# Performance work log

Measured on AMD Instinct MI355X. Metric: run time of the kernel, lower is better.

The kernel has to match this reference:

```python
import jax, jax.numpy as jnp
import numpy as np

SPARSITY = 0.01
NUM_BLOCKS = 8

def _softshrink(v, lam):
    return jnp.sign(v) * jnp.maximum(jnp.abs(v) - lam, 0.0)

def setup_inputs() -> dict:
    key = jax.random.key(0)
    ks = jax.random.split(key, 5)
    B, H, W, C = 4, 128, 128, 768
    nb, bs = NUM_BLOCKS, C // NUM_BLOCKS
    return {
        "x": jax.random.normal(ks[0], (B, H, W, C), dtype=jnp.float32),
        "w1": jax.random.normal(ks[1], (2, nb, bs, bs), dtype=jnp.float32) * 0.02,
        "b1": jax.random.normal(ks[2], (2, nb, bs), dtype=jnp.float32) * 0.02,
        "w2": jax.random.normal(ks[3], (2, nb, bs, bs), dtype=jnp.float32) * 0.02,
        "b2": jax.random.normal(ks[4], (2, nb, bs), dtype=jnp.float32) * 0.02,
    }

def reference(x, w1, b1, w2, b2):
    B, H, W, C = x.shape
    nb = NUM_BLOCKS
    bs = C // nb
    # FFT token mixing (ortho-normalized), real->complex half-spectrum
    xf = jnp.fft.rfft2(x, axes=(1, 2), norm="ortho")  # [B, H, W//2+1, C]
    Hf, Wf = xf.shape[1], xf.shape[2]
    xr = xf.real.reshape(B, Hf, Wf, nb, bs)
    xi = xf.imag.reshape(B, Hf, Wf, nb, bs)
    # kept_modes = H*W//2+1 with hard_thresholding_fraction=1 >= Wf -> all modes kept
    # Block-diagonal complex MLP layer 1 + GELU (exact, matching torch nn.GELU)
    o1r = jax.nn.gelu(
        jnp.einsum("bhwni,nio->bhwno", xr, w1[0])
        - jnp.einsum("bhwni,nio->bhwno", xi, w1[1]) + b1[0],
        approximate=False)
    o1i = jax.nn.gelu(
        jnp.einsum("bhwni,nio->bhwno", xi, w1[0])
        + jnp.einsum("bhwni,nio->bhwno", xr, w1[1]) + b1[1],
        approximate=False)
    # Layer 2 (complex matmul), then softshrink on real/imag parts
    o2r = (jnp.einsum("bhwni,nio->bhwno", o1r, w2[0])
           - jnp.einsum("bhwni,nio->bhwno", o1i, w2[1]) + b2[0])
    o2i = (jnp.einsum("bhwni,nio->bhwno", o1i, w2[0])
           + jnp.einsum("bhwni,nio->bhwno", o1r, w2[1]) + b2[1])
    o2r = _softshrink(o2r, SPARSITY)
    o2i = _softshrink(o2i, SPARSITY)
    xc = (o2r + 1j * o2i).reshape(B, Hf, Wf, C)
    out = jnp.fft.irfft2(xc, s=(H, W), axes=(1, 2), norm="ortho")
    return out
```

## Files before the change

### kernel.cpp

```cpp
#include <hip/hip_runtime.h>
#include <hip/hip_bf16.h>
#include <math.h>

typedef __bf16 bfx8 __attribute__((ext_vector_type(8)));
typedef __bf16 bfx4 __attribute__((ext_vector_type(4)));
typedef float f32x4 __attribute__((ext_vector_type(4)));

__device__ __forceinline__ int bitrev7(int x) {
  return ((x & 1) << 6) | ((x & 2) << 4) | ((x & 4) << 2) | (x & 8)
       | ((x & 16) >> 2) | ((x & 32) >> 4) | ((x & 64) >> 6);
}

__device__ __forceinline__ void bfly(float& ar, float& ai, float& br, float& bi,
                                     float tc, float ts) {
  float dr = ar - br, di = ai - bi;
  ar += br; ai += bi;
  br = dr * tc - di * ts;
  bi = dr * ts + di * tc;
}

__device__ __forceinline__ void build_tw(float2* tw, float sign, int tid) {
  if (tid < 64) {
    float s_, c_;
    __sincosf(sign * (float)(2.0 * M_PI / 128.0) * (float)tid, &s_, &c_);
    tw[tid] = make_float2(c_, s_);
  }
}

__device__ __forceinline__ void fft_stages04(float (&xr)[4][8], float (&xi)[4][8],
                                             const float2* tw, int wq) {
  #pragma unroll
  for (int a = 0; a < 8; ++a) {
    #pragma unroll
    for (int b = 0; b < 2; ++b) {
      float2 t = tw[wq + 4 * a + 32 * b];
      bfly(xr[b][a], xi[b][a], xr[b + 2][a], xi[b + 2][a], t.x, t.y);
    }
  }
  #pragma unroll
  for (int a = 0; a < 8; ++a) {
    float2 t = tw[2 * (wq + 4 * a)];
    bfly(xr[0][a], xi[0][a], xr[1][a], xi[1][a], t.x, t.y);
    bfly(xr[2][a], xi[2][a], xr[3][a], xi[3][a], t.x, t.y);
  }
  #pragma unroll
  for (int a = 0; a < 4; ++a) {
    float2 t = tw[4 * (wq + 4 * a)];
    #pragma unroll
    for (int b = 0; b < 4; ++b)
      bfly(xr[b][a], xi[b][a], xr[b][a + 4], xi[b][a + 4], t.x, t.y);
  }
  {
    float2 t0 = tw[8 * wq];
    float2 t1 = tw[8 * (wq + 4)];
    #pragma unroll
    for (int b = 0; b < 4; ++b) {
      bfly(xr[b][0], xi[b][0], xr[b][2], xi[b][2], t0.x, t0.y);
      bfly(xr[b][1], xi[b][1], xr[b][3], xi[b][3], t1.x, t1.y);
      bfly(xr[b][4], xi[b][4], xr[b][6], xi[b][6], t0.x, t0.y);
      bfly(xr[b][5], xi[b][5], xr[b][7], xi[b][7], t1.x, t1.y);
    }
  }
  {
    float2 t = tw[16 * wq];
    #pragma unroll
    for (int b = 0; b < 4; ++b) {
      #pragma unroll
      for (int a = 0; a < 8; a += 2)
        bfly(xr[b][a], xi[b][a], xr[b][a + 1], xi[b][a + 1], t.x, t.y);
    }
  }
}

__device__ __forceinline__ void fft_stages56(float (&yr)[4], float (&yi)[4], float sign) {
  float dr, di;
  dr = yr[0] - yr[2]; di = yi[0] - yi[2];
  yr[0] += yr[2]; yi[0] += yi[2]; yr[2] = dr; yi[2] = di;
  dr = yr[1] - yr[3]; di = yi[1] - yi[3];
  yr[1] += yr[3]; yi[1] += yi[3];
  yr[3] = -sign * di; yi[3] = sign * dr;
  dr = yr[0] - yr[1]; di = yi[0] - yi[1];
  yr[0] += yr[1]; yi[0] += yi[1]; yr[1] = dr; yi[1] = di;
  dr = yr[2] - yr[3]; di = yi[2] - yi[3];
  yr[2] += yr[3]; yi[2] += yi[3]; yr[3] = dr; yi[3] = di;
}

__global__ __launch_bounds__(256, 2) void k_fftw_fwd(
    const float* __restrict__ x, float* __restrict__ Xr, float* __restrict__ Xi) {
  __shared__ float2 l[128 * 64];
  __shared__ float2 tw[64];
  const int bh = blockIdx.x;
  const int c0 = blockIdx.y * 64;
  const int tid = threadIdx.x;
  const int c = tid & 63, wq = tid >> 6;
  build_tw(tw, -1.f, tid);
  const float* xrow = x + (size_t)bh * (128 * 768) + c0 + c;
  float xr[4][8], xi_[4][8];
  #pragma unroll
  for (int b = 0; b < 4; ++b)
    #pragma unroll
    for (int a = 0; a < 8; ++a) {
      int p = wq + 4 * a + 32 * b;
      xr[b][a] = xrow[(size_t)p * 768];
      xi_[b][a] = 0.f;
    }
  __syncthreads();
  fft_stages04(xr, xi_, tw, wq);
  #pragma unroll
  for (int b = 0; b < 4; ++b)
    #pragma unroll
    for (int a = 0; a < 8; ++a) {
      int p = wq + 4 * a + 32 * b;
      l[p * 64 + c] = make_float2(xr[b][a], xi_[b][a]);
    }
  __syncthreads();
  const float sc = 1.f / 128.f;
  #pragma unroll
  for (int t = 0; t < 8; ++t) {
    int g = wq + 4 * t;
    float yr[4], yi[4];
    #pragma unroll
    for (int d = 0; d < 4; ++d) {
      float2 v = l[(4 * g + d) * 64 + c];
      yr[d] = v.x; yi[d] = v.y;
    }
    fft_stages56(yr, yi, -1.f);
    #pragma unroll
    for (int d = 0; d < 4; ++d) {
      int f = bitrev7(4 * g + d);
      if (f < 65) {
        Xr[((size_t)bh * 65 + f) * 768 + c0 + c]  = yr[d] * sc;
        Xi[((size_t)bh * 128 + f) * 768 + c0 + c] = yi[d] * sc;
      }
    }
  }
}

__global__ __launch_bounds__(256, 2) void k_ffth(
    float* Xr, float* Xi, float sign, float scale) {
  __shared__ float2 l[128 * 64];
  __shared__ float2 tw[64];
  const int bw = blockIdx.x;
  const int b = bw / 65, wf = bw % 65;
  const int c0 = blockIdx.y * 64;
  const int tid = threadIdx.x;
  const int c = tid & 63, wq = tid >> 6;
  build_tw(tw, sign, tid);
  const size_t baser = ((size_t)b * 128 * 65 + wf) * 768 + c0 + c;
  const size_t basei = ((size_t)b * 128 * 128 + wf) * 768 + c0 + c;
  float xr[4][8], xi_[4][8];
  #pragma unroll
  for (int bb = 0; bb < 4; ++bb)
    #pragma unroll
    for (int a = 0; a < 8; ++a) {
      int p = wq + 4 * a + 32 * bb;
      xr[bb][a]  = Xr[baser + (size_t)p * (65 * 768)];
      xi_[bb][a] = Xi[basei + (size_t)p * (128 * 768)];
    }
  __syncthreads();
  fft_stages04(xr, xi_, tw, wq);
  #pragma unroll
  for (int bb = 0; bb < 4; ++bb)
    #pragma unroll
    for (int a = 0; a < 8; ++a) {
      int p = wq + 4 * a + 32 * bb;
      l[p * 64 + c] = make_float2(xr[bb][a], xi_[bb][a]);
    }
  __syncthreads();
  #pragma unroll
  for (int t = 0; t < 8; ++t) {
    int g = wq + 4 * t;
    float yr[4], yi[4];
    #pragma unroll
    for (int d = 0; d < 4; ++d) {
      float2 v = l[(4 * g + d) * 64 + c];
      yr[d] = v.x; yi[d] = v.y;
    }
    fft_stages56(yr, yi, sign);
    #pragma unroll
    for (int d = 0; d < 4; ++d) {
      int hf = bitrev7(4 * g + d);
      Xr[baser + (size_t)hf * (65 * 768)]  = yr[d] * scale;
      Xi[basei + (size_t)hf * (128 * 768)] = yi[d] * scale;
    }
  }
}

#define MP 104
__device__ __forceinline__ bfx8 neg8(bfx8 v) {
  union { bfx8 b; unsigned int u[4]; } t;
  t.b = v;
  t.u[0] ^= 0x80008000u; t.u[1] ^= 0x80008000u;
  t.u[2] ^= 0x80008000u; t.u[3] ^= 0x80008000u;
  return t.b;
}

__global__ __launch_bounds__(256, 2) void k_mlp(
    float* __restrict__ Xr, float* __restrict__ Xi,
    const float* __restrict__ w1, const float* __restrict__ b1,
    const float* __restrict__ w2, const float* __restrict__ b2) {
  __shared__ __align__(16) __bf16 Xl[2][64][MP];
  __shared__ __align__(16) __bf16 Wl[2][96][MP];
  const int n = blockIdx.y;
  const int m0 = blockIdx.x * 64;
  const int tid = threadIdx.x;
  const int lane = tid & 63;
  const int w = tid >> 6;
  const int col = lane & 15;
  const int quad = lane >> 4;

  for (int e = tid; e < 64 * 24; e += 256) {
    int mm = e / 24, k4 = (e % 24) * 4;
    int m = m0 + mm;
    int bh = m / 65, wf = m - bh * 65;
    const float4 vr = *(const float4*)&Xr[(size_t)m * 768 + n * 96 + k4];
    const float4 vi = *(const float4*)&Xi[((size_t)bh * 128 + wf) * 768 + n * 96 + k4];
    bfx4 br = { (__bf16)vr.x, (__bf16)vr.y, (__bf16)vr.z, (__bf16)vr.w };
    bfx4 bi = { (__bf16)vi.x, (__bf16)vi.y, (__bf16)vi.z, (__bf16)vi.w };
    *(bfx4*)&Xl[0][mm][k4] = br;
    *(bfx4*)&Xl[1][mm][k4] = bi;
  }
  for (int e = tid; e < 2 * 96 * 24; e += 256) {
    int ri = e / (96 * 24);
    int r = e - ri * (96 * 24);
    int kin = r / 24, oc4 = (r - kin * 24) * 4;
    const float4 v = *(const float4*)&w1[(size_t)ri * 73728 + ((size_t)n * 96 + kin) * 96 + oc4];
    Wl[ri][oc4 + 0][kin] = (__bf16)v.x;
    Wl[ri][oc4 + 1][kin] = (__bf16)v.y;
    Wl[ri][oc4 + 2][kin] = (__bf16)v.z;
    Wl[ri][oc4 + 3][kin] = (__bf16)v.w;
  }
  __syncthreads();

  const f32x4 fz = { 0.f, 0.f, 0.f, 0.f };
  f32x4 accR[6], accI[6];
  #pragma unroll
  for (int ct = 0; ct < 6; ++ct) { accR[ct] = fz; accI[ct] = fz; }

  const int mrow = w * 16 + col;
  #pragma unroll
  for (int kc = 0; kc < 3; ++kc) {
    const int kb = kc * 32 + quad * 8;
    bfx8 axr = *(const bfx8*)&Xl[0][mrow][kb];
    bfx8 axi = *(const bfx8*)&Xl[1][mrow][kb];
    bfx8 axin = neg8(axi);
    #pragma unroll
    for (int ct = 0; ct < 6; ++ct) {
      bfx8 bwr = *(const bfx8*)&Wl[0][ct * 16 + col][kb];
      bfx8 bwi = *(const bfx8*)&Wl[1][ct * 16 + col][kb];
      accR[ct] = __builtin_amdgcn_mfma_f32_16x16x32_bf16(axr,  bwr, accR[ct], 0, 0, 0);
      accR[ct] = __builtin_amdgcn_mfma_f32_16x16x32_bf16(axin, bwi, accR[ct], 0, 0, 0);
      accI[ct] = __builtin_amdgcn_mfma_f32_16x16x32_bf16(axi,  bwr, accI[ct], 0, 0, 0);
      accI[ct] = __builtin_amdgcn_mfma_f32_16x16x32_bf16(axr,  bwi, accI[ct], 0, 0, 0);
    }
  }
  __syncthreads();

  #pragma unroll
  for (int ct = 0; ct < 6; ++ct) {
    int oc = ct * 16 + col;
    float br = b1[n * 96 + oc];
    float bi = b1[768 + n * 96 + oc];
    int mbase = w * 16 + quad * 4;
    #pragma unroll
    for (int r = 0; r < 4; ++r) {
      float vr = accR[ct][r] + br;
      float vi = accI[ct][r] + bi;
      vr = 0.5f * vr * (1.f + erff(vr * 0.70710678118654752f));
      vi = 0.5f * vi * (1.f + erff(vi * 0.70710678118654752f));
      Xl[0][mbase + r][oc] = (__bf16)vr;
      Xl[1][mbase + r][oc] = (__bf16)vi;
    }
  }
  for (int e = tid; e < 2 * 96 * 24; e += 256) {
    int ri = e / (96 * 24);
    int r = e - ri * (96 * 24);
    int kin = r / 24, oc4 = (r - kin * 24) * 4;
    const float4 v = *(const float4*)&w2[(size_t)ri * 73728 + ((size_t)n * 96 + kin) * 96 + oc4];
    Wl[ri][oc4 + 0][kin] = (__bf16)v.x;
    Wl[ri][oc4 + 1][kin] = (__bf16)v.y;
    Wl[ri][oc4 + 2][kin] = (__bf16)v.z;
    Wl[ri][oc4 + 3][kin] = (__bf16)v.w;
  }
  __syncthreads();

  #pragma unroll
  for (int ct = 0; ct < 6; ++ct) { accR[ct] = fz; accI[ct] = fz; }
  #pragma unroll
  for (int kc = 0; kc < 3; ++kc) {
    const int kb = kc * 32 + quad * 8;
    bfx8 axr = *(const bfx8*)&Xl[0][mrow][kb];
    bfx8 axi = *(const bfx8*)&Xl[1][mrow][kb];
    bfx8 axin = neg8(axi);
    #pragma unroll
    for (int ct = 0; ct < 6; ++ct) {
      bfx8 bwr = *(const bfx8*)&Wl[0][ct * 16 + col][kb];
      bfx8 bwi = *(const bfx8*)&Wl[1][ct * 16 + col][kb];
      accR[ct] = __builtin_amdgcn_mfma_f32_16x16x32_bf16(axr,  bwr, accR[ct], 0, 0, 0);
      accR[ct] = __builtin_amdgcn_mfma_f32_16x16x32_bf16(axin, bwi, accR[ct], 0, 0, 0);
      accI[ct] = __builtin_amdgcn_mfma_f32_16x16x32_bf16(axi,  bwr, accI[ct], 0, 0, 0);
      accI[ct] = __builtin_amdgcn_mfma_f32_16x16x32_bf16(axr,  bwi, accI[ct], 0, 0, 0);
    }
  }

  #pragma unroll
  for (int ct = 0; ct < 6; ++ct) {
    int oc = ct * 16 + col;
    float br = b2[n * 96 + oc];
    float bi = b2[768 + n * 96 + oc];
    #pragma unroll
    for (int r = 0; r < 4; ++r) {
      int m = m0 + w * 16 + quad * 4 + r;
      int bh = m / 65, wf = m - bh * 65;
      float vr = accR[ct][r] + br;
      float vi = accI[ct][r] + bi;
      vr = (vr > 0.01f) ? vr - 0.01f : ((vr < -0.01f) ? vr + 0.01f : 0.f);
      vi = (vi > 0.01f) ? vi - 0.01f : ((vi < -0.01f) ? vi + 0.01f : 0.f);
      Xr[(size_t)m * 768 + n * 96 + oc] = vr;
      Xi[((size_t)bh * 128 + wf) * 768 + n * 96 + oc] = vi;
    }
  }
}

__global__ __launch_bounds__(256, 2) void k_ifftw(
    const float* __restrict__ Xr, float* io) {
  __shared__ float2 l[128 * 64];
  __shared__ float2 tw[64];
  const int bh = blockIdx.x;
  const int c0 = blockIdx.y * 64;
  const int tid = threadIdx.x;
  const int c = tid & 63, wq = tid >> 6;
  build_tw(tw, +1.f, tid);
  float xr[4][8], xi_[4][8];
  #pragma unroll
  for (int b = 0; b < 4; ++b)
    #pragma unroll
    for (int a = 0; a < 8; ++a) {
      int p = wq + 4 * a + 32 * b;
      int src = (p <= 64) ? p : 128 - p;
      float sg = (p <= 64) ? 1.f : -1.f;
      xr[b][a]  = Xr[((size_t)bh * 65 + src) * 768 + c0 + c];
      xi_[b][a] = sg * io[((size_t)bh * 128 + src) * 768 + c0 + c];
    }
  __syncthreads();
  fft_stages04(xr, xi_, tw, wq);
  #pragma unroll
  for (int b = 0; b < 4; ++b)
    #pragma unroll
    for (int a = 0; a < 8; ++a) {
      int p = wq + 4 * a + 32 * b;
      l[p * 64 + c] = make_float2(xr[b][a], xi_[b][a]);
    }
  __syncthreads();
  #pragma unroll
  for (int t = 0; t < 8; ++t) {
    int g = wq + 4 * t;
    float yr[4], yi[4];
    #pragma unroll
    for (int d = 0; d < 4; ++d) {
      float2 v = l[(4 * g + d) * 64 + c];
      yr[d] = v.x; yi[d] = v.y;
    }
    fft_stages56(yr, yi, +1.f);
    #pragma unroll
    for (int d = 0; d < 4; ++d) {
      int w = bitrev7(4 * g + d);
      io[((size_t)bh * 128 + w) * 768 + c0 + c] = yr[d];
    }
  }
}

extern "C" void kernel_launch(void* const* d_in, const int* in_sizes, int n_in,
                              void* d_out, int out_size, void* d_ws, size_t ws_size,
                              hipStream_t stream) {
  const float* x  = (const float*)d_in[0];
  const float* w1 = (const float*)d_in[1];
  const float* b1 = (const float*)d_in[2];
  const float* w2 = (const float*)d_in[3];
  const float* b2 = (const float*)d_in[4];
  float* out = (float*)d_out;
  float* Xr = (float*)d_ws;
  float* Xi = out;

  dim3 blk(256);
  k_fftw_fwd<<<dim3(512, 12), blk, 0, stream>>>(x, Xr, Xi);
  k_ffth   <<<dim3(260, 12), blk, 0, stream>>>(Xr, Xi, -1.f, 1.f);
  k_mlp    <<<dim3(520, 8),  blk, 0, stream>>>(Xr, Xi, w1, b1, w2, b2);
  k_ffth   <<<dim3(260, 12), blk, 0, stream>>>(Xr, Xi, +1.f, 1.f / 128.f);
  k_ifftw  <<<dim3(512, 12), blk, 0, stream>>>(Xr, out);
}
```

Measured before the change: 836.8 us.

## Pre-transpose weights to bf16 once and stream MLP operands from global memory

Adds a small prep kernel that converts w1/w2 to bf16 in a transposed [n][oc][kin] layout. It stores them in unused padding rows of the output buffer (Xi's rows w=65..127). The MLP kernel then reads X and weights straight from global/L2 into MFMA registers instead of staging both in shared memory. Only the GELU intermediate stays in a smaller XOR-swizzled LDS tile, which drops most __syncthreads and raises occupancy to 4 blocks per CU. The costs are more global loads per wave, an extra launch, and reliance on those padding rows staying unused until the MLP finishes and later kernels overwrite them.

```diff
diff --git a/kernel.cpp b/kernel.cpp
--- a/kernel.cpp
+++ b/kernel.cpp
@@ -186,7 +186,26 @@
   }
 }
 
-#define MP 104
+__global__ void k_wprep(const float* __restrict__ w1, const float* __restrict__ w2,
+                        float* __restrict__ out) {
+  int e = blockIdx.x * 256 + threadIdx.x;
+  int kin8 = e % 12;
+  int t = e / 12;
+  int oc = t % 96;
+  int t2 = t / 96;
+  int n = t2 & 7;
+  int q = t2 >> 3;
+  int L = q >> 1, ri = q & 1;
+  const float* src = (L ? w2 : w1) + (size_t)ri * 73728 + ((size_t)n * 96) * 96 + oc;
+  bfx8 v;
+  #pragma unroll
+  for (int j = 0; j < 8; ++j)
+    v[j] = (__bf16)src[(size_t)(kin8 * 8 + j) * 96];
+  __bf16* wt = (__bf16*)(out + ((size_t)q * 128 + 65) * 768);
+  *(bfx8*)&wt[((size_t)(n * 96 + oc)) * 96 + kin8 * 8] = v;
+}
+
+#define MPB 208
 __device__ __forceinline__ bfx8 neg8(bfx8 v) {
   union { bfx8 b; unsigned int u[4]; } t;
   t.b = v;
@@ -195,12 +214,12 @@
   return t.b;
 }
 
-__global__ __launch_bounds__(256, 2) void k_mlp(
+__global__ __launch_bounds__(256, 4) void k_mlp(
     float* __restrict__ Xr, float* __restrict__ Xi,
-    const float* __restrict__ w1, const float* __restrict__ b1,
-    const float* __restrict__ w2, const float* __restrict__ b2) {
-  __shared__ __align__(16) __bf16 Xl[2][64][MP];
-  __shared__ __align__(16) __bf16 Wl[2][96][MP];
+    const __bf16* __restrict__ wt0,
+    const float* __restrict__ b1, const float* __restrict__ b2) {
+  __shared__ __align__(16) unsigned char O1[2 * 64 * MPB];
+
   const int n = blockIdx.y;
   const int m0 = blockIdx.x * 64;
   const int tid = threadIdx.x;
@@ -208,94 +227,79 @@
   const int w = tid >> 6;
   const int col = lane & 15;
   const int quad = lane >> 4;
-
-  for (int e = tid; e < 64 * 24; e += 256) {
-    int mm = e / 24, k4 = (e % 24) * 4;
-    int m = m0 + mm;
-    int bh = m / 65, wf = m - bh * 65;
-    const float4 vr = *(const float4*)&Xr[(size_t)m * 768 + n * 96 + k4];
-    const float4 vi = *(const float4*)&Xi[((size_t)bh * 128 + wf) * 768 + n * 96 + k4];
-    bfx4 br = { (__bf16)vr.x, (__bf16)vr.y, (__bf16)vr.z, (__bf16)vr.w };
-    bfx4 bi = { (__bf16)vi.x, (__bf16)vi.y, (__bf16)vi.z, (__bf16)vi.w };
-    *(bfx4*)&Xl[0][mm][k4] = br;
-    *(bfx4*)&Xl[1][mm][k4] = bi;
-  }
-  for (int e = tid; e < 2 * 96 * 24; e += 256) {
-    int ri = e / (96 * 24);
-    int r = e - ri * (96 * 24);
-    int kin = r / 24, oc4 = (r - kin * 24) * 4;
-    const float4 v = *(const float4*)&w1[(size_t)ri * 73728 + ((size_t)n * 96 + kin) * 96 + oc4];
-    Wl[ri][oc4 + 0][kin] = (__bf16)v.x;
-    Wl[ri][oc4 + 1][kin] = (__bf16)v.y;
-    Wl[ri][oc4 + 2][kin] = (__bf16)v.z;
-    Wl[ri][oc4 + 3][kin] = (__bf16)v.w;
-  }
-  __syncthreads();
+  const int mrow = w * 16 + col;
+  const int m = m0 + mrow;
+  const int bh = m / 65, wf = m - bh * 65;
+  const size_t xr_base = (size_t)m * 768 + n * 96;
+  const size_t xi_base = ((size_t)bh * 128 + wf) * 768 + n * 96;
+  const __bf16* w1r = wt0 + (size_t)n * 9216;
+  const __bf16* w1i = w1r + 196608;
+  const __bf16* w2r = w1r + 2 * 196608;
+  const __bf16* w2i = w1r + 3 * 196608;
 
   const f32x4 fz = { 0.f, 0.f, 0.f, 0.f };
   f32x4 accR[6], accI[6];
   #pragma unroll
   for (int ct = 0; ct < 6; ++ct) { accR[ct] = fz; accI[ct] = fz; }
 
-  const int mrow = w * 16 + col;
   #pragma unroll
   for (int kc = 0; kc < 3; ++kc) {
     const int kb = kc * 32 + quad * 8;
-    bfx8 axr = *(const bfx8*)&Xl[0][mrow][kb];
-    bfx8 axi = *(const bfx8*)&Xl[1][mrow][kb];
+    float4 vr0 = *(const float4*)&Xr[xr_base + kb];
+    float4 vr1 = *(const float4*)&Xr[xr_base + kb + 4];
+    float4 vi0 = *(const float4*)&Xi[xi_base + kb];
+    float4 vi1 = *(const float4*)&Xi[xi_base + kb + 4];
+    bfx8 axr = { (__bf16)vr0.x, (__bf16)vr0.y, (__bf16)vr0.z, (__bf16)vr0.w,
+                 (__bf16)vr1.x, (__bf16)vr1.y, (__bf16)vr1.z, (__bf16)vr1.w };
+    bfx8 axi = { (__bf16)vi0.x, (__bf16)vi0.y, (__bf16)vi0.z, (__bf16)vi0.w,
+                 (__bf16)vi1.x, (__bf16)vi1.y, (__bf16)vi1.z, (__bf16)vi1.w };
     bfx8 axin = neg8(axi);
     #pragma unroll
     for (int ct = 0; ct < 6; ++ct) {
-      bfx8 bwr = *(const bfx8*)&Wl[0][ct * 16 + col][kb];
-      bfx8 bwi = *(const bfx8*)&Wl[1][ct * 16 + col][kb];
+      const size_t wb = (size_t)(ct * 16 + col) * 96 + kb;
+      bfx8 bwr = *(const bfx8*)&w1r[wb];
+      bfx8 bwi = *(const bfx8*)&w1i[wb];
       accR[ct] = __builtin_amdgcn_mfma_f32_16x16x32_bf16(axr,  bwr, accR[ct], 0, 0, 0);
       accR[ct] = __builtin_amdgcn_mfma_f32_16x16x32_bf16(axin, bwi, accR[ct], 0, 0, 0);
       accI[ct] = __builtin_amdgcn_mfma_f32_16x16x32_bf16(axi,  bwr, accI[ct], 0, 0, 0);
       accI[ct] = __builtin_amdgcn_mfma_f32_16x16x32_bf16(axr,  bwi, accI[ct], 0, 0, 0);
     }
   }
-  __syncthreads();
 
   #pragma unroll
   for (int ct = 0; ct < 6; ++ct) {
     int oc = ct * 16 + col;
     float br = b1[n * 96 + oc];
     float bi = b1[768 + n * 96 + oc];
-    int mbase = w * 16 + quad * 4;
     #pragma unroll
     for (int r = 0; r < 4; ++r) {
+      int row = w * 16 + quad * 4 + r;
       float vr = accR[ct][r] + br;
       float vi = accI[ct][r] + bi;
       vr = 0.5f * vr * (1.f + erff(vr * 0.70710678118654752f));
       vi = 0.5f * vi * (1.f + erff(vi * 0.70710678118654752f));
-      Xl[0][mbase + r][oc] = (__bf16)vr;
-      Xl[1][mbase + r][oc] = (__bf16)vi;
-    }
-  }
-  for (int e = tid; e < 2 * 96 * 24; e += 256) {
-    int ri = e / (96 * 24);
-    int r = e - ri * (96 * 24);
-    int kin = r / 24, oc4 = (r - kin * 24) * 4;
-    const float4 v = *(const float4*)&w2[(size_t)ri * 73728 + ((size_t)n * 96 + kin) * 96 + oc4];
-    Wl[ri][oc4 + 0][kin] = (__bf16)v.x;
-    Wl[ri][oc4 + 1][kin] = (__bf16)v.y;
-    Wl[ri][oc4 + 2][kin] = (__bf16)v.z;
-    Wl[ri][oc4 + 3][kin] = (__bf16)v.w;
-  }
-  __syncthreads();
+      int mask = ((row >> 2) & 3) << 4;
+      *(__bf16*)&O1[row * MPB + ((oc * 2) ^ mask)]             = (__bf16)vr;
+      *(__bf16*)&O1[64 * MPB + row * MPB + ((oc * 2) ^ mask)]  = (__bf16)vi;
+    }
+  }
+  asm volatile("s_waitcnt lgkmcnt(0)" ::: "memory");
 
   #pragma unroll
   for (int ct = 0; ct < 6; ++ct) { accR[ct] = fz; accI[ct] = fz; }
+  const int amask = ((mrow >> 2) & 3) << 4;
   #pragma unroll
   for (int kc = 0; kc < 3; ++kc) {
     const int kb = kc * 32 + quad * 8;
-    bfx8 axr = *(const bfx8*)&Xl[0][mrow][kb];
-    bfx8 axi = *(const bfx8*)&Xl[1][mrow][kb];
+    const int bc = (kb * 2) ^ amask;
+    bfx8 axr = *(const bfx8*)&O1[mrow * MPB + bc];
+    bfx8 axi = *(const bfx8*)&O1[64 * MPB + mrow * MPB + bc];
     bfx8 axin = neg8(axi);
     #pragma unroll
     for (int ct = 0; ct < 6; ++ct) {
-      bfx8 bwr = *(const bfx8*)&Wl[0][ct * 16 + col][kb];
-      bfx8 bwi = *(const bfx8*)&Wl[1][ct * 16 + col][kb];
+      const size_t wb = (size_t)(ct * 16 + col) * 96 + kb;
+      bfx8 bwr = *(const bfx8*)&w2r[wb];
+      bfx8 bwi = *(const bfx8*)&w2i[wb];
       accR[ct] = __builtin_amdgcn_mfma_f32_16x16x32_bf16(axr,  bwr, accR[ct], 0, 0, 0);
       accR[ct] = __builtin_amdgcn_mfma_f32_16x16x32_bf16(axin, bwi, accR[ct], 0, 0, 0);
       accI[ct] = __builtin_amdgcn_mfma_f32_16x16x32_bf16(axi,  bwr, accI[ct], 0, 0, 0);
@@ -310,14 +314,14 @@
     float bi = b2[768 + n * 96 + oc];
     #pragma unroll
     for (int r = 0; r < 4; ++r) {
-      int m = m0 + w * 16 + quad * 4 + r;
-      int bh = m / 65, wf = m - bh * 65;
+      int mm = m0 + w * 16 + quad * 4 + r;
+      int bh2 = mm / 65, wf2 = mm - bh2 * 65;
       float vr = accR[ct][r] + br;
       float vi = accI[ct][r] + bi;
       vr = (vr > 0.01f) ? vr - 0.01f : ((vr < -0.01f) ? vr + 0.01f : 0.f);
       vi = (vi > 0.01f) ? vi - 0.01f : ((vi < -0.01f) ? vi + 0.01f : 0.f);
-      Xr[(size_t)m * 768 + n * 96 + oc] = vr;
-      Xi[((size_t)bh * 128 + wf) * 768 + n * 96 + oc] = vi;
+      Xr[(size_t)mm * 768 + n * 96 + oc] = vr;
+      Xi[((size_t)bh2 * 128 + wf2) * 768 + n * 96 + oc] = vi;
     }
   }
 }
@@ -381,11 +385,13 @@
   float* out = (float*)d_out;
   float* Xr = (float*)d_ws;
   float* Xi = out;
+  const __bf16* wt0 = (const __bf16*)(out + (size_t)65 * 768);
 
   dim3 blk(256);
+  k_wprep  <<<dim3(144),      blk, 0, stream>>>(w1, w2, out);
   k_fftw_fwd<<<dim3(512, 12), blk, 0, stream>>>(x, Xr, Xi);
-  k_ffth   <<<dim3(260, 12), blk, 0, stream>>>(Xr, Xi, -1.f, 1.f);
-  k_mlp    <<<dim3(520, 8),  blk, 0, stream>>>(Xr, Xi, w1, b1, w2, b2);
-  k_ffth   <<<dim3(260, 12), blk, 0, stream>>>(Xr, Xi, +1.f, 1.f / 128.f);
-  k_ifftw  <<<dim3(512, 12), blk, 0, stream>>>(Xr, out);
-}
+  k_ffth   <<<dim3(260, 12),  blk, 0, stream>>>(Xr, Xi, -1.f, 1.f);
+  k_mlp    <<<dim3(520, 8),   blk, 0, stream>>>(Xr, Xi, wt0, b1, b2);
+  k_ffth   <<<dim3(260, 12),  blk, 0, stream>>>(Xr, Xi, +1.f, 1.f / 128.f);
+  k_ifftw  <<<dim3(512, 12),  blk, 0, stream>>>(Xr, out);
+}
```

Result: faster. 750.4 us (-10.3%).
